# Performance work log

Measured on AMD Instinct MI355X. Metric: run time of the kernel, lower is better.

The kernel has to match this reference:

```python
import jax, jax.numpy as jnp
import numpy as np

K = 1024      # num_embeddings
D = 256       # embedding_dim
BETA = 0.25
DECAY = 0.99
EPS = 1e-05


def setup_inputs() -> dict:
    key = jax.random.key(0)
    k1, k2 = jax.random.split(key)
    z_e = jax.random.normal(k1, (32, D, 32, 32), dtype=jnp.float32)
    embedding = jax.random.normal(k2, (K, D), dtype=jnp.float32)
    ema_cluster_size = jnp.zeros((K,), dtype=jnp.float32)
    ema_w = embedding  # buffer initialized as a clone of the codebook
    return {"z_e": z_e, "embedding": embedding,
            "ema_cluster_size": ema_cluster_size, "ema_w": ema_w}


def reference(z_e, embedding, ema_cluster_size, ema_w):
    B, Dd, H, W = z_e.shape
    # (B, D, H, W) -> (N, D)
    flat_z = jnp.transpose(z_e, (0, 2, 3, 1)).reshape(-1, Dd)

    # L2 distance argmin (||z||^2 + ||e||^2 - 2 z.e)
    dist = (jnp.sum(flat_z * flat_z, axis=1, keepdims=True)
            + jnp.sum(embedding * embedding, axis=1)
            - 2.0 * flat_z @ embedding.T)
    indices = jnp.argmin(dist, axis=1)  # (N,)

    # EMA update (operates on detached values; buffers updated in-place in torch)
    flat_z_sg = jax.lax.stop_gradient(flat_z)
    cluster_size = jax.ops.segment_sum(
        jnp.ones_like(indices, dtype=z_e.dtype), indices, num_segments=K)
    new_ema_cluster_size = DECAY * ema_cluster_size + (1.0 - DECAY) * cluster_size
    dw = jax.ops.segment_sum(flat_z_sg, indices, num_segments=K)  # one_hot.T @ flat_z
    new_ema_w = DECAY * ema_w + (1.0 - DECAY) * dw
    new_embedding = new_ema_w / (new_ema_cluster_size + EPS)[:, None]

    # Gather uses the *updated* codebook (torch copies into the buffer first)
    z_q_flat = new_embedding[indices]                      # (N, D)
    z_q = jnp.transpose(z_q_flat.reshape(B, H, W, Dd), (0, 3, 1, 2))

    # Straight-through estimator + commitment loss
    z_q_st = z_e + jax.lax.stop_gradient(z_q - z_e)
    vq_loss = BETA * jnp.mean((z_e - jax.lax.stop_gradient(z_q)) ** 2)

    return (z_q_st, vq_loss, indices.reshape(B, H, W),
            new_embedding, new_ema_cluster_size, new_ema_w)
```

## Files before the change

### kernel.cpp

```cpp
#include <hip/hip_runtime.h>
#include <stdint.h>

#define N_ROWS 32768
#define K_CODES 1024
#define D_DIM 256
#define NELEM 8388608

#define WS_COUNTS 0
#define WS_LOSS 1030
#define WS_ENORM 263168
#define WS_ROWBEST_BYTES 1056768
#define WS_IDX_BYTES 1318912

#define O_ZQ 0
#define O_LOSS 8388608
#define O_IDX 8388609
#define O_EMB 8421377
#define O_CS 8683521
#define O_EMAW 8684545

#define EP_BYTE_OFF 33685520

typedef _Float16 half8 __attribute__((ext_vector_type(8)));
typedef float f32x16 __attribute__((ext_vector_type(16)));

__device__ __forceinline__ unsigned int fenc(float f) {
    unsigned int u = __float_as_uint(f);
    return (u & 0x80000000u) ? ~u : (u | 0x80000000u);
}
__device__ __forceinline__ unsigned long long umin64(unsigned long long a, unsigned long long b) {
    return a < b ? a : b;
}
__device__ __forceinline__ void gll16(const void* g, void* l) {
    __builtin_amdgcn_global_load_lds((const __attribute__((address_space(1))) void*)g,
                                     (__attribute__((address_space(3))) void*)l, 16, 0, 0);
}

__global__ __launch_bounds__(256) void k_conv_e(const float* __restrict__ emb,
                                                _Float16* __restrict__ Ep,
                                                float* __restrict__ enorm,
                                                float* __restrict__ ws) {
    int k = blockIdx.x, d = threadIdx.x;
    int gid = k * 256 + d;
    if (gid < 2048) ws[gid] = 0.0f;
    unsigned long long* rb = (unsigned long long*)((char*)ws + WS_ROWBEST_BYTES);
    if (gid < N_ROWS) rb[gid] = 0xFFFFFFFFFFFFFFFFull;

    float v = emb[k * 256 + d];
    _Float16 h = (_Float16)v;
    _Float16 l = (_Float16)(v - (float)h);
    int s = d >> 3, sub = d & 7;
    Ep[((size_t)s * 1024 + k) * 8 + sub] = h;
    Ep[((size_t)(32 + s) * 1024 + k) * 8 + sub] = l;
    float sq = v * v;
    #pragma unroll
    for (int off = 32; off >= 1; off >>= 1) sq += __shfl_down(sq, off, 64);
    __shared__ float red[4];
    if ((d & 63) == 0) red[d >> 6] = sq;
    __syncthreads();
    if (d == 0) enorm[k] = (red[0] + red[1]) + (red[2] + red[3]);
}

__global__ __launch_bounds__(256) void k_conv_z(const float* __restrict__ z_e,
                                                _Float16* __restrict__ Zp,
                                                float* __restrict__ lossacc) {
    __shared__ float lt[64 * 68];
    __shared__ float red[4];
    int t = threadIdx.x;
    int hw0 = blockIdx.x * 64, d0 = blockIdx.y * 64, b = blockIdx.z;
    const float* src = z_e + (size_t)b * 262144 + (size_t)d0 * 1024 + hw0;
    int dl = t >> 4, hl = (t & 15) * 4;
    float sq = 0.0f;
    #pragma unroll
    for (int i = 0; i < 4; i++) {
        int d = dl + i * 16;
        float4 v = *(const float4*)(src + (size_t)d * 1024 + hl);
        sq += v.x * v.x + v.y * v.y + v.z * v.z + v.w * v.w;
        lt[(hl + 0) * 68 + d] = v.x;
        lt[(hl + 1) * 68 + d] = v.y;
        lt[(hl + 2) * 68 + d] = v.z;
        lt[(hl + 3) * 68 + d] = v.w;
    }
    __syncthreads();
    int hr = t >> 2, seg = t & 3;
    int n = b * 1024 + hw0 + hr;
    int sg0 = (d0 >> 3) + seg * 2;
    half8 hi[2], lo[2];
    #pragma unroll
    for (int p = 0; p < 2; p++) {
        #pragma unroll
        for (int j = 0; j < 8; j++) {
            float v = lt[hr * 68 + seg * 16 + p * 8 + j];
            _Float16 h = (_Float16)v;
            hi[p][j] = h;
            lo[p][j] = (_Float16)(v - (float)h);
        }
    }
    *(half8*)(Zp + ((size_t)(sg0 + 0) * 32768 + n) * 8) = hi[0];
    *(half8*)(Zp + ((size_t)(sg0 + 1) * 32768 + n) * 8) = hi[1];
    *(half8*)(Zp + ((size_t)(32 + sg0) * 32768 + n) * 8) = lo[0];
    *(half8*)(Zp + ((size_t)(33 + sg0) * 32768 + n) * 8) = lo[1];
    #pragma unroll
    for (int off = 32; off >= 1; off >>= 1) sq += __shfl_down(sq, off, 64);
    if ((t & 63) == 0) red[t >> 6] = sq;
    __syncthreads();
    if (t == 0) atomicAdd(lossacc, (red[0] + red[1]) + (red[2] + red[3]));
}

__global__ __launch_bounds__(512) void k_mm(const _Float16* __restrict__ Zp,
                                            const _Float16* __restrict__ Ep,
                                            const float* __restrict__ enorm,
                                            unsigned long long* __restrict__ row_best) {
    __shared__ __align__(16) char smem[65536];

    int t = threadIdx.x;
    int lane = t & 63, wv = t >> 6;
    int b = blockIdx.x;
    int wgid = (b & 7) * 64 + (b >> 3);
    int rt = wgid >> 2;
    int ct = wgid & 3;
    int row0 = rt * 256, code0 = ct * 256;

    int wr = wv >> 2, wc = wv & 3;
    int m31 = lane & 31, ko = lane >> 5;

    f32x16 acc[4][2];
    #pragma unroll
    for (int m = 0; m < 4; m++)
        #pragma unroll
        for (int n = 0; n < 2; n++)
            #pragma unroll
            for (int r = 0; r < 16; r++) acc[m][n][r] = 0.0f;

    int sseg_st = wv >> 1;
    int rowbase = (wv & 1) * 128;
    const char* zgw = (const char*)Zp + ((size_t)row0 + rowbase + lane) * 16;
    const char* egw = (const char*)Ep + ((size_t)code0 + rowbase + lane) * 16;

    auto zsb = [](int tt) { return (tt < 16 ? tt : tt - 16) * 4; };
    auto esb = [](int tt) { return tt < 8 ? tt * 4 : (tt < 16 ? (tt - 8) * 4 : 32 + (tt - 16) * 4); };

    auto STAGE = [&](int c, int buf) {
        int zs = zsb(c) + sseg_st, es = esb(c) + sseg_st;
        const char* zg = zgw + (size_t)zs * 32768 * 16;
        const char* eg = egw + (size_t)es * 1024 * 16;
        char* zl = smem + buf * 32768 + sseg_st * 4096 + rowbase * 16;
        char* el = smem + buf * 32768 + 16384 + sseg_st * 4096 + rowbase * 16;
        gll16(zg, zl);
        gll16(zg + 64 * 16, zl + 64 * 16);
        gll16(eg, el);
        gll16(eg + 64 * 16, el + 64 * 16);
    };

    STAGE(0, 0);
    STAGE(1, 1);
    asm volatile("s_waitcnt vmcnt(4)" ::: "memory");
    __builtin_amdgcn_s_barrier();
    asm volatile("" ::: "memory");

    for (int c = 0; c < 24; c++) {
        const _Float16* Za = (const _Float16*)(smem + (c & 1) * 32768);
        const _Float16* Ea = (const _Float16*)(smem + (c & 1) * 32768 + 16384);
        __builtin_amdgcn_s_setprio(1);
        #pragma unroll
        for (int ks = 0; ks < 2; ks++) {
            int sseg = 2 * ks + ko;
            half8 a0 = *(const half8*)(Za + (sseg * 256 + wr * 128 +  0 + m31) * 8);
            half8 a1 = *(const half8*)(Za + (sseg * 256 + wr * 128 + 32 + m31) * 8);
            half8 a2 = *(const half8*)(Za + (sseg * 256 + wr * 128 + 64 + m31) * 8);
            half8 a3 = *(const half8*)(Za + (sseg * 256 + wr * 128 + 96 + m31) * 8);
            half8 b0 = *(const half8*)(Ea + (sseg * 256 + wc * 64 +  0 + m31) * 8);
            half8 b1 = *(const half8*)(Ea + (sseg * 256 + wc * 64 + 32 + m31) * 8);
            acc[0][0] = __builtin_amdgcn_mfma_f32_32x32x16_f16(a0, b0, acc[0][0], 0, 0, 0);
            acc[0][1] = __builtin_amdgcn_mfma_f32_32x32x16_f16(a0, b1, acc[0][1], 0, 0, 0);
            acc[1][0] = __builtin_amdgcn_mfma_f32_32x32x16_f16(a1, b0, acc[1][0], 0, 0, 0);
            acc[1][1] = __builtin_amdgcn_mfma_f32_32x32x16_f16(a1, b1, acc[1][1], 0, 0, 0);
            acc[2][0] = __builtin_amdgcn_mfma_f32_32x32x16_f16(a2, b0, acc[2][0], 0, 0, 0);
            acc[2][1] = __builtin_amdgcn_mfma_f32_32x32x16_f16(a2, b1, acc[2][1], 0, 0, 0);
            acc[3][0] = __builtin_amdgcn_mfma_f32_32x32x16_f16(a3, b0, acc[3][0], 0, 0, 0);
            acc[3][1] = __builtin_amdgcn_mfma_f32_32x32x16_f16(a3, b1, acc[3][1], 0, 0, 0);
        }
        __builtin_amdgcn_s_setprio(0);
        asm volatile("s_waitcnt lgkmcnt(0)" ::: "memory");
        __builtin_amdgcn_s_barrier();
        if (c < 22) STAGE(c + 2, c & 1);
        if (c < 23) {
            if (c < 22) asm volatile("s_waitcnt vmcnt(4)" ::: "memory");
            else        asm volatile("s_waitcnt vmcnt(0)" ::: "memory");
            __builtin_amdgcn_s_barrier();
            asm volatile("" ::: "memory");
        }
    }

    unsigned long long* slot = (unsigned long long*)smem;
    float en0 = enorm[code0 + wc * 64 + m31];
    float en1 = enorm[code0 + wc * 64 + 32 + m31];
    unsigned int col0 = code0 + wc * 64 + m31;
    unsigned int col1 = col0 + 32;

    if (wc == 0) {
        #pragma unroll
        for (int m = 0; m < 4; m++)
            #pragma unroll
            for (int j = 0; j < 16; j++) {
                int row = wr * 128 + m * 32 + 4 * ko + (j & 3) + 8 * (j >> 2);
                unsigned long long p0 = ((unsigned long long)fenc(en0 - 2.0f * acc[m][0][j]) << 32) | col0;
                unsigned long long p1 = ((unsigned long long)fenc(en1 - 2.0f * acc[m][1][j]) << 32) | col1;
                slot[row * 32 + ((m31 + row) & 31)] = umin64(p0, p1);
            }
    }
    __syncthreads();
    if (wc != 0) {
        #pragma unroll
        for (int m = 0; m < 4; m++)
            #pragma unroll
            for (int j = 0; j < 16; j++) {
                int row = wr * 128 + m * 32 + 4 * ko + (j & 3) + 8 * (j >> 2);
                unsigned long long p0 = ((unsigned long long)fenc(en0 - 2.0f * acc[m][0][j]) << 32) | col0;
                unsigned long long p1 = ((unsigned long long)fenc(en1 - 2.0f * acc[m][1][j]) << 32) | col1;
                atomicMin(&slot[row * 32 + ((m31 + row) & 31)], umin64(p0, p1));
            }
    }
    __syncthreads();
    if (t < 256) {
        unsigned long long mm = slot[t * 32 + (t & 31)];
        #pragma unroll
        for (int i = 1; i < 32; i++) mm = umin64(mm, slot[t * 32 + ((i + t) & 31)]);
        atomicMin(&row_best[row0 + t], mm);
    }
}

__global__ __launch_bounds__(256) void k_fin_idx(const unsigned long long* __restrict__ rb,
                                                 int* __restrict__ idxs,
                                                 float* __restrict__ counts,
                                                 float* __restrict__ out) {
    __shared__ float hist[K_CODES];
    int t = threadIdx.x;
    #pragma unroll
    for (int j = 0; j < 4; j++) hist[j * 256 + t] = 0.0f;
    __syncthreads();
    int i = blockIdx.x * 256 + t;
    int id = (int)(rb[i] & 0xFFFFFFFFull);
    idxs[i] = id;
    out[O_IDX + i] = (float)id;
    atomicAdd(&hist[id], 1.0f);
    __syncthreads();
    #pragma unroll
    for (int j = 0; j < 4; j++) {
        float h = hist[j * 256 + t];
        if (h != 0.0f) atomicAdd(&counts[j * 256 + t], h);
    }
}

__global__ __launch_bounds__(512) void k_dw(const float* __restrict__ z_e,
                                            const int* __restrict__ idxs,
                                            float* __restrict__ dw) {
    __shared__ float acc[2 * K_CODES];
    int t = threadIdx.x;
    int d = blockIdx.x;
    #pragma unroll
    for (int j = 0; j < 4; j++) acc[j * 512 + t] = 0.0f;
    __syncthreads();
    int rep = (t & 1) * K_CODES;
    for (int b = 0; b < 32; b++) {
        int2 id2 = *(const int2*)(idxs + b * 1024 + t * 2);
        float2 v = *(const float2*)(z_e + (size_t)b * 262144 + (size_t)d * 1024 + t * 2);
        atomicAdd(&acc[rep + id2.x], v.x);
        atomicAdd(&acc[rep + id2.y], v.y);
    }
    __syncthreads();
    float* pr = dw + (size_t)d * 1024;
    #pragma unroll
    for (int j = 0; j < 2; j++) pr[j * 512 + t] = acc[j * 512 + t] + acc[K_CODES + j * 512 + t];
}

__global__ __launch_bounds__(256) void k_red(const float* __restrict__ dw,
                                             const float* __restrict__ ema_cs,
                                             const float* __restrict__ ema_w,
                                             const float* __restrict__ counts,
                                             float* __restrict__ lossacc,
                                             float* __restrict__ out) {
    __shared__ float tile[64 * 69];
    __shared__ float csl[64];
    __shared__ float craw[64];
    __shared__ float red[4];
    int t = threadIdx.x;
    int k0 = blockIdx.x * 64, d0 = blockIdx.y * 64;
    int dr = t >> 4, kc = t & 15;
    if (t < 64) {
        float c = counts[k0 + t];
        craw[t] = c;
        csl[t] = 0.99f * ema_cs[k0 + t] + 0.01f * c;
    }
    #pragma unroll
    for (int q = 0; q < 4; q++) {
        float4 v = *(const float4*)(dw + (size_t)(d0 + dr + 16 * q) * 1024 + k0 + kc * 4);
        float* p = tile + (dr + 16 * q) * 69 + kc * 4;
        p[0] = v.x; p[1] = v.y; p[2] = v.z; p[3] = v.w;
    }
    __syncthreads();
    int kk = t >> 2, dq = t & 3;
    int k = k0 + kk;
    float inv = 1.0f / (csl[kk] + 1e-5f);
    float cr = craw[kk];
    float lterm = 0.0f;
    #pragma unroll
    for (int j4 = 0; j4 < 4; j4++) {
        int dd = dq * 16 + j4 * 4;
        size_t kd = (size_t)k * 256 + d0 + dd;
        float4 w = *(const float4*)(ema_w + kd);
        float s0 = tile[(dd + 0) * 69 + kk];
        float s1 = tile[(dd + 1) * 69 + kk];
        float s2 = tile[(dd + 2) * 69 + kk];
        float s3 = tile[(dd + 3) * 69 + kk];
        float4 nw;
        nw.x = 0.99f * w.x + 0.01f * s0;
        nw.y = 0.99f * w.y + 0.01f * s1;
        nw.z = 0.99f * w.z + 0.01f * s2;
        nw.w = 0.99f * w.w + 0.01f * s3;
        *(float4*)(out + O_EMAW + kd) = nw;
        float4 ne = {nw.x * inv, nw.y * inv, nw.z * inv, nw.w * inv};
        *(float4*)(out + O_EMB + kd) = ne;
        lterm += ne.x * (cr * ne.x - 2.0f * s0);
        lterm += ne.y * (cr * ne.y - 2.0f * s1);
        lterm += ne.z * (cr * ne.z - 2.0f * s2);
        lterm += ne.w * (cr * ne.w - 2.0f * s3);
    }
    if (blockIdx.y == 0 && t < 64) out[O_CS + k0 + t] = csl[t];
    #pragma unroll
    for (int off = 32; off >= 1; off >>= 1) lterm += __shfl_down(lterm, off, 64);
    if ((t & 63) == 0) red[t >> 6] = lterm;
    __syncthreads();
    if (t == 0) atomicAdd(lossacc, (red[0] + red[1]) + (red[2] + red[3]));
}

__global__ __launch_bounds__(256) void k_bcast(const int* __restrict__ idxs,
                                               const float* __restrict__ lossacc,
                                               float* __restrict__ out) {
    __shared__ float lt[64 * 68];
    __shared__ int sid[64];
    int t = threadIdx.x;
    int hw0 = blockIdx.x * 64, d0 = blockIdx.y * 64, b = blockIdx.z;
    if (t < 64) sid[t] = idxs[b * 1024 + hw0 + t];
    __syncthreads();
    int r = t >> 2, c = t & 3;
    const float* nrow = out + O_EMB + (size_t)sid[r] * 256 + d0;
    #pragma unroll
    for (int it = 0; it < 4; it++) {
        int dd = it * 16 + c * 4;
        float4 q = *(const float4*)(nrow + dd);
        float* p = lt + r * 68 + dd;
        p[0] = q.x; p[1] = q.y; p[2] = q.z; p[3] = q.w;
    }
    __syncthreads();
    int dl = t >> 4, hl = (t & 15) * 4;
    float* dst = out + O_ZQ + (size_t)b * 262144 + (size_t)d0 * 1024 + hw0;
    #pragma unroll
    for (int i = 0; i < 4; i++) {
        int d = dl + i * 16;
        float4 w;
        w.x = lt[(hl + 0) * 68 + d];
        w.y = lt[(hl + 1) * 68 + d];
        w.z = lt[(hl + 2) * 68 + d];
        w.w = lt[(hl + 3) * 68 + d];
        *(float4*)(dst + (size_t)d * 1024 + hl) = w;
    }
    if (blockIdx.x == 0 && blockIdx.y == 0 && blockIdx.z == 0 && t == 0)
        out[O_LOSS] = lossacc[0] * 2.9802322387695312e-08f;
}

extern "C" void kernel_launch(void* const* d_in, const int* in_sizes, int n_in,
                              void* d_out, int out_size, void* d_ws, size_t ws_size,
                              hipStream_t stream) {
    const float* z_e = (const float*)d_in[0];
    const float* emb = (const float*)d_in[1];
    const float* ema_cs = (const float*)d_in[2];
    const float* ema_w = (const float*)d_in[3];
    float* out = (float*)d_out;
    float* ws = (float*)d_ws;

    float* counts = ws + WS_COUNTS;
    float* lossacc = ws + WS_LOSS;
    float* enorm = ws + WS_ENORM;
    unsigned long long* row_best = (unsigned long long*)((char*)d_ws + WS_ROWBEST_BYTES);
    int* idxs = (int*)((char*)d_ws + WS_IDX_BYTES);

    _Float16* Zp = (_Float16*)d_out;
    _Float16* Ep = (_Float16*)((char*)d_out + EP_BYTE_OFF);
    float* dw = (float*)d_out;

    k_conv_e<<<1024, 256, 0, stream>>>(emb, Ep, enorm, ws);
    k_conv_z<<<dim3(16, 4, 32), 256, 0, stream>>>(z_e, Zp, lossacc);
    k_mm<<<512, 512, 0, stream>>>(Zp, Ep, enorm, row_best);
    k_fin_idx<<<128, 256, 0, stream>>>(row_best, idxs, counts, out);
    k_dw<<<256, 512, 0, stream>>>(z_e, idxs, dw);
    k_red<<<dim3(16, 4), 256, 0, stream>>>(dw, ema_cs, ema_w, counts, lossacc, out);
    k_bcast<<<dim3(16, 4, 32), 256, 0, stream>>>(idxs, lossacc, out);
}
```

Baseline: 236.3 us.

## Restructure split-fp16 distance GEMM into 8 larger stages with fused hi/lo MFMAs

Replaces the 24-chunk pipeline, where hi and lo K-segments were staged as separate chunks, with 8 stages that each load the Z-hi, Z-lo, E-hi and E-lo slices together into a 128KB double-buffered LDS area. Each warp group now stages one operand quadrant, and the three split-precision MFMAs per tile pair are issued back to back from registers. The aim is fewer barriers and waitcnt round-trips, with more MFMAs between syncs. The cost is double the LDS footprint, which likely limits occupancy to one block per CU, plus more live registers for the eight operand fragments.

Measured after the change: 237.2 us. About the same (+0.4%).

```diff
diff --git a/kernel.cpp b/kernel.cpp
--- a/kernel.cpp
+++ b/kernel.cpp
@@ -111,7 +111,7 @@
                                             const _Float16* __restrict__ Ep,
                                             const float* __restrict__ enorm,
                                             unsigned long long* __restrict__ row_best) {
-    __shared__ __align__(16) char smem[65536];
+    __shared__ __align__(16) char smem[131072];
 
     int t = threadIdx.x;
     int lane = t & 63, wv = t >> 6;
@@ -132,61 +132,67 @@
             #pragma unroll
             for (int r = 0; r < 16; r++) acc[m][n][r] = 0.0f;
 
-    int sseg_st = wv >> 1;
-    int rowbase = (wv & 1) * 128;
-    const char* zgw = (const char*)Zp + ((size_t)row0 + rowbase + lane) * 16;
-    const char* egw = (const char*)Ep + ((size_t)code0 + rowbase + lane) * 16;
-
-    auto zsb = [](int tt) { return (tt < 16 ? tt : tt - 16) * 4; };
-    auto esb = [](int tt) { return tt < 8 ? tt * 4 : (tt < 16 ? (tt - 8) * 4 : 32 + (tt - 16) * 4); };
-
-    auto STAGE = [&](int c, int buf) {
-        int zs = zsb(c) + sseg_st, es = esb(c) + sseg_st;
-        const char* zg = zgw + (size_t)zs * 32768 * 16;
-        const char* eg = egw + (size_t)es * 1024 * 16;
-        char* zl = smem + buf * 32768 + sseg_st * 4096 + rowbase * 16;
-        char* el = smem + buf * 32768 + 16384 + sseg_st * 4096 + rowbase * 16;
-        gll16(zg, zl);
-        gll16(zg + 64 * 16, zl + 64 * 16);
-        gll16(eg, el);
-        gll16(eg + 64 * 16, el + 64 * 16);
+    int quad = wv & 3, half = wv >> 2;
+    bool isZ = (quad & 2) == 0;
+    int lobias = (quad & 1) ? 32 : 0;
+    size_t gstride = isZ ? (size_t)32768 * 16 : (size_t)1024 * 16;
+    const char* gsel = isZ
+        ? (const char*)Zp + ((size_t)row0 + half * 128 + lane) * 16
+        : (const char*)Ep + ((size_t)code0 + half * 128 + lane) * 16;
+    char* lbase = smem + quad * 16384 + (half * 128) * 16;
+
+    auto STAGE = [&](int g, int buf) {
+        #pragma unroll
+        for (int s = 0; s < 4; s++) {
+            const char* src = gsel + (size_t)(lobias + 4 * g + s) * gstride;
+            char* dst = lbase + buf * 65536 + s * 4096;
+            gll16(src, dst);
+            gll16(src + 64 * 16, dst + 64 * 16);
+        }
     };
 
     STAGE(0, 0);
     STAGE(1, 1);
-    asm volatile("s_waitcnt vmcnt(4)" ::: "memory");
+    asm volatile("s_waitcnt vmcnt(8)" ::: "memory");
     __builtin_amdgcn_s_barrier();
     asm volatile("" ::: "memory");
 
-    for (int c = 0; c < 24; c++) {
-        const _Float16* Za = (const _Float16*)(smem + (c & 1) * 32768);
-        const _Float16* Ea = (const _Float16*)(smem + (c & 1) * 32768 + 16384);
+    for (int g = 0; g < 8; g++) {
+        const _Float16* zh = (const _Float16*)(smem + (g & 1) * 65536);
+        const _Float16* zl = zh + 8192;
+        const _Float16* eh = zh + 16384;
+        const _Float16* el = zh + 24576;
         __builtin_amdgcn_s_setprio(1);
         #pragma unroll
         for (int ks = 0; ks < 2; ks++) {
             int sseg = 2 * ks + ko;
-            half8 a0 = *(const half8*)(Za + (sseg * 256 + wr * 128 +  0 + m31) * 8);
-            half8 a1 = *(const half8*)(Za + (sseg * 256 + wr * 128 + 32 + m31) * 8);
-            half8 a2 = *(const half8*)(Za + (sseg * 256 + wr * 128 + 64 + m31) * 8);
-            half8 a3 = *(const half8*)(Za + (sseg * 256 + wr * 128 + 96 + m31) * 8);
-            half8 b0 = *(const half8*)(Ea + (sseg * 256 + wc * 64 +  0 + m31) * 8);
-            half8 b1 = *(const half8*)(Ea + (sseg * 256 + wc * 64 + 32 + m31) * 8);
-            acc[0][0] = __builtin_amdgcn_mfma_f32_32x32x16_f16(a0, b0, acc[0][0], 0, 0, 0);
-            acc[0][1] = __builtin_amdgcn_mfma_f32_32x32x16_f16(a0, b1, acc[0][1], 0, 0, 0);
-            acc[1][0] = __builtin_amdgcn_mfma_f32_32x32x16_f16(a1, b0, acc[1][0], 0, 0, 0);
-            acc[1][1] = __builtin_amdgcn_mfma_f32_32x32x16_f16(a1, b1, acc[1][1], 0, 0, 0);
-            acc[2][0] = __builtin_amdgcn_mfma_f32_32x32x16_f16(a2, b0, acc[2][0], 0, 0, 0);
-            acc[2][1] = __builtin_amdgcn_mfma_f32_32x32x16_f16(a2, b1, acc[2][1], 0, 0, 0);
-            acc[3][0] = __builtin_amdgcn_mfma_f32_32x32x16_f16(a3, b0, acc[3][0], 0, 0, 0);
-            acc[3][1] = __builtin_amdgcn_mfma_f32_32x32x16_f16(a3, b1, acc[3][1], 0, 0, 0);
+            half8 azh[4], azl[4], beh[2], bel[2];
+            #pragma unroll
+            for (int i = 0; i < 4; i++) {
+                azh[i] = *(const half8*)(zh + (sseg * 256 + wr * 128 + 32 * i + m31) * 8);
+                azl[i] = *(const half8*)(zl + (sseg * 256 + wr * 128 + 32 * i + m31) * 8);
+            }
+            #pragma unroll
+            for (int j = 0; j < 2; j++) {
+                beh[j] = *(const half8*)(eh + (sseg * 256 + wc * 64 + 32 * j + m31) * 8);
+                bel[j] = *(const half8*)(el + (sseg * 256 + wc * 64 + 32 * j + m31) * 8);
+            }
+            #pragma unroll
+            for (int i = 0; i < 4; i++)
+                #pragma unroll
+                for (int j = 0; j < 2; j++) {
+                    acc[i][j] = __builtin_amdgcn_mfma_f32_32x32x16_f16(azh[i], beh[j], acc[i][j], 0, 0, 0);
+                    acc[i][j] = __builtin_amdgcn_mfma_f32_32x32x16_f16(azl[i], beh[j], acc[i][j], 0, 0, 0);
+                    acc[i][j] = __builtin_amdgcn_mfma_f32_32x32x16_f16(azh[i], bel[j], acc[i][j], 0, 0, 0);
+                }
         }
         __builtin_amdgcn_s_setprio(0);
         asm volatile("s_waitcnt lgkmcnt(0)" ::: "memory");
         __builtin_amdgcn_s_barrier();
-        if (c < 22) STAGE(c + 2, c & 1);
-        if (c < 23) {
-            if (c < 22) asm volatile("s_waitcnt vmcnt(4)" ::: "memory");
-            else        asm volatile("s_waitcnt vmcnt(0)" ::: "memory");
+        if (g < 6) STAGE(g + 2, g & 1);
+        if (g < 7) {
+            if (g < 6) asm volatile("s_waitcnt vmcnt(8)" ::: "memory");
+            else       asm volatile("s_waitcnt vmcnt(0)" ::: "memory");
             __builtin_amdgcn_s_barrier();
             asm volatile("" ::: "memory");
         }
```
